# Kernel tuning notes

Hardware: AMD Instinct MI355X
Metric: run time of the kernel (lower is better)

## Reference

```python
import jax, jax.numpy as jnp
import numpy as np

N_NODES = 100000
N_EDGES = 1200000
F_IN, F_HID, F_OUT = 128, 64, 40


def gcn_conv(x, W, b, src, dst, n):
    # PyG GCNConv: h = x @ W; add self-loops; symmetric norm; scatter-add; + bias
    h = x @ W  # [N, F]
    loops = jnp.arange(n)
    s = jnp.concatenate([src, loops])
    d = jnp.concatenate([dst, loops])
    deg = jnp.zeros((n,), x.dtype).at[d].add(jnp.asarray(1.0, x.dtype))
    dis = jax.lax.rsqrt(deg)  # deg >= 1 thanks to self-loops
    norm = dis[s] * dis[d]  # [E+N]
    msg = h[s] * norm[:, None]  # gather + scale
    out = jnp.zeros((n, h.shape[1]), x.dtype).at[d].add(msg)  # scatter-add
    return out + b


def setup_inputs() -> dict:
    key = jax.random.key(0)
    ks = jax.random.split(key, 8)
    sc = lambda f: 1.0 / np.sqrt(f)
    return {
        "x": jax.random.normal(ks[0], (N_NODES, F_IN), jnp.float32),
        "edge_index": jax.random.randint(ks[1], (2, N_EDGES), 0, N_NODES, jnp.int64),
        "W1": jax.random.normal(ks[2], (F_IN, F_HID), jnp.float32) * sc(F_IN),
        "b1": jnp.zeros((F_HID,), jnp.float32),
        "W2": jax.random.normal(ks[3], (F_HID, F_HID), jnp.float32) * sc(F_HID),
        "b2": jnp.zeros((F_HID,), jnp.float32),
        "W3": jax.random.normal(ks[4], (F_HID, F_OUT), jnp.float32) * sc(F_HID),
        "b3": jnp.zeros((F_OUT,), jnp.float32),
    }


def reference(x, edge_index, W1, b1, W2, b2, W3, b3):
    src, dst = edge_index[0], edge_index[1]
    n = x.shape[0]
    h = jax.nn.relu(gcn_conv(x, W1, b1, src, dst, n))  # dropout is identity (eval)
    h = jax.nn.relu(gcn_conv(h, W2, b2, src, dst, n))
    out = gcn_conv(h, W3, b3, src, dst, n)
    return jax.nn.log_softmax(out, axis=1)
```

## Files before the change

### kernel.cpp

```cpp
#include <hip/hip_runtime.h>
#include <math.h>


static inline int cdiv(long a, int b) { return (int)((a + b - 1) / b); }

__device__ __forceinline__ unsigned short f2bf(float f) {
    unsigned u = __float_as_uint(f);
    u += 0x7fffu + ((u >> 16) & 1u);
    return (unsigned short)(u >> 16);
}
__device__ __forceinline__ float bf2f(unsigned short b) {
    return __uint_as_float(((unsigned)b) << 16);
}

typedef float floatx2 __attribute__((ext_vector_type(2)));
__device__ __forceinline__ float4 fp8x4_f(unsigned u) {
    floatx2 lo = __builtin_amdgcn_cvt_pk_f32_fp8(u, false);
    floatx2 hi = __builtin_amdgcn_cvt_pk_f32_fp8(u, true);
    float4 r; r.x = lo[0]; r.y = lo[1]; r.z = hi[0]; r.w = hi[1];
    return r;
}
__device__ __forceinline__ unsigned f_fp8x4(float4 v) {
    unsigned r = 0;
    r = __builtin_amdgcn_cvt_pk_fp8_f32(v.x, v.y, r, false);
    r = __builtin_amdgcn_cvt_pk_fp8_f32(v.z, v.w, r, true);
    return r;
}

#define RSH 9
#define RNODES 512
#define GB 1024
#define NBMAX 256
#define SMASK 0x1FFFF
#define PSLACK (RNODES * 16)

__global__ __launch_bounds__(256)
void k_bhist(const int* __restrict__ dst, int* __restrict__ bh,
             int E, int NB, int EPB) {
    __shared__ int bcnt[NBMAX];
    const int tid = threadIdx.x, blk = blockIdx.x;
    for (int i = tid; i < NB; i += 256) bcnt[i] = 0;
    __syncthreads();
    const int e1 = min(E, (blk + 1) * EPB);
    for (int e = blk * EPB + tid; e < e1; e += 256)
        atomicAdd(&bcnt[dst[e] >> RSH], 1);
    __syncthreads();
    for (int i = tid; i < NB; i += 256) bh[i * GB + blk] = bcnt[i];
}

__global__ __launch_bounds__(256)
void k_bscatter(const int* __restrict__ src, const int* __restrict__ dst,
                const int* __restrict__ eoff, int* __restrict__ ebuf,
                int E, int NB, int EPB) {
    __shared__ int cur[NBMAX];
    const int tid = threadIdx.x, blk = blockIdx.x;
    for (int i = tid; i < NB; i += 256) cur[i] = eoff[i * GB + blk];
    __syncthreads();
    const int e1 = min(E, (blk + 1) * EPB);
    for (int e = blk * EPB + tid; e < e1; e += 256) {
        int d = dst[e];
        int s = src[e];
        int pos = atomicAdd(&cur[d >> RSH], 1);
        ebuf[pos] = ((d & (RNODES - 1)) << 17) | s;
    }
}

__global__ __launch_bounds__(1024)
void k_csr(const int* __restrict__ ebuf, const int* __restrict__ eoff,
           uint2* __restrict__ rpd, float* __restrict__ dis,
           unsigned int* __restrict__ esrcb, int N, int E, int NB) {
    __shared__ int cnt[RNODES];
    __shared__ int cur[RNODES];
    __shared__ int sm[1024];
    const int tid = threadIdx.x, b = blockIdx.x;
    const int node0 = b << RSH;
    const int bb = eoff[b * GB];
    const int be = (b + 1 == NB) ? E : eoff[(b + 1) * GB];
    const int pbase = ((bb + 15) & ~15) + b * PSLACK;

    if (tid < RNODES) cnt[tid] = 0;
    __syncthreads();
    for (int e = bb + tid; e < be; e += 1024)
        atomicAdd(&cnt[ebuf[e] >> 17], 1);
    __syncthreads();

    int v  = (tid < RNODES) ? cnt[tid] : 0;
    int pv = (v + 15) & ~15;
    sm[tid] = pv;
    __syncthreads();
    for (int off = 1; off < RNODES; off <<= 1) {
        int t = (tid >= off) ? sm[tid - off] : 0;
        __syncthreads();
        sm[tid] += t;
        __syncthreads();
    }
    if (tid < RNODES) {
        int excl = sm[tid] - pv;
        cur[tid] = pbase + excl;
        int node = node0 + tid;
        if (node < N) {
            rpd[node] = make_uint2((unsigned)(pbase + excl), (unsigned)((v + 15) >> 4));
            dis[node] = rsqrtf(1.0f + (float)v);
        }
    }
    __syncthreads();
    const int ptot = sm[RNODES - 1];

    const unsigned ZOFF = (unsigned)N << 6;
    for (int k = tid; k < ptot; k += 1024) esrcb[pbase + k] = ZOFF;
    __syncthreads();

    for (int e = bb + tid; e < be; e += 1024) {
        int ev = ebuf[e];
        int slot = atomicAdd(&cur[ev >> 17], 1);
        esrcb[slot] = (unsigned)(ev & SMASK) << 6;
    }
}

#define SCAN_B 1024
__global__ void k_scan1(const int* __restrict__ cnt, int* __restrict__ rp,
                        int* __restrict__ bsum, int n, char* __restrict__ zbase,
                        int N) {
    __shared__ int sm[SCAN_B];
    const int tid = threadIdx.x;
    const int gid = blockIdx.x * SCAN_B + tid;
    if (blockIdx.x == 0 && tid < 16)
        ((unsigned*)(zbase + (size_t)N * 64))[tid] = 0;
    int v = (gid < n) ? cnt[gid] : 0;
    sm[tid] = v;
    __syncthreads();
    for (int off = 1; off < SCAN_B; off <<= 1) {
        int t = (tid >= off) ? sm[tid - off] : 0;
        __syncthreads();
        sm[tid] += t;
        __syncthreads();
    }
    if (gid < n) rp[gid] = sm[tid] - v;
    if (tid == SCAN_B - 1) bsum[blockIdx.x] = sm[tid];
}

__global__ void k_scan2(int* __restrict__ bsum, int nb) {
    __shared__ int sm[SCAN_B];
    const int tid = threadIdx.x;
    int v = (tid < nb) ? bsum[tid] : 0;
    sm[tid] = v;
    __syncthreads();
    for (int off = 1; off < SCAN_B; off <<= 1) {
        int t = (tid >= off) ? sm[tid - off] : 0;
        __syncthreads();
        sm[tid] += t;
        __syncthreads();
    }
    if (tid < nb) bsum[tid] = sm[tid] - v;
}

__global__ void k_scan3(int* __restrict__ rp, const int* __restrict__ bsum, int n, int E) {
    const int gid = blockIdx.x * SCAN_B + threadIdx.x;
    if (gid < n) rp[gid] += bsum[gid / SCAN_B];
    if (gid == n) rp[n] = E;
}

__device__ __forceinline__ void fma4(float a, const float4& w, float4& acc) {
    acc.x = fmaf(a, w.x, acc.x);
    acc.y = fmaf(a, w.y, acc.y);
    acc.z = fmaf(a, w.z, acc.z);
    acc.w = fmaf(a, w.w, acc.w);
}

template<int K, bool BF16IN, int MINW>
__global__ __launch_bounds__(256, MINW)
void k_gemm_lds(const void* __restrict__ Xv, const float* __restrict__ W,
                const float* __restrict__ dis, void* __restrict__ Hout, int N) {
    constexpr int KP = K + 4;
    __shared__ float xs[64 * KP];
    __shared__ float wsh[K * 64];
    const int tid = threadIdx.x;
    const int tx = tid & 15;
    const int ty = tid >> 4;
    const int row0 = blockIdx.x * 64;

    {
        const float4* Wg = (const float4*)W;
        float4* Wl = (float4*)wsh;
#pragma unroll
        for (int i = 0; i < K * 16 / 256; ++i)
            Wl[i * 256 + tid] = Wg[i * 256 + tid];
    }
    {
        constexpr int F4 = K / 4;
        for (int i = tid; i < 64 * F4; i += 256) {
            int r = i / F4, c = i - r * F4;
            int gr = min(row0 + r, N - 1);
            float4 v;
            if (BF16IN) {
                ushort4 u = *(const ushort4*)((const unsigned short*)Xv + (size_t)gr * K + c * 4);
                v.x = bf2f(u.x); v.y = bf2f(u.y); v.z = bf2f(u.z); v.w = bf2f(u.w);
            } else {
                v = *(const float4*)((const float*)Xv + (size_t)gr * K + c * 4);
            }
            *(float4*)(xs + r * KP + c * 4) = v;
        }
    }
    __syncthreads();

    float4 acc0 = {0.f, 0.f, 0.f, 0.f};
    float4 acc1 = {0.f, 0.f, 0.f, 0.f};
    float4 acc2 = {0.f, 0.f, 0.f, 0.f};
    float4 acc3 = {0.f, 0.f, 0.f, 0.f};

    const float* xr0 = xs + (ty * 4 + 0) * KP;
    const float* xr1 = xs + (ty * 4 + 1) * KP;
    const float* xr2 = xs + (ty * 4 + 2) * KP;
    const float* xr3 = xs + (ty * 4 + 3) * KP;

#pragma unroll 2
    for (int k = 0; k < K; k += 4) {
        float4 w0 = *(const float4*)(wsh + (k + 0) * 64 + tx * 4);
        float4 w1 = *(const float4*)(wsh + (k + 1) * 64 + tx * 4);
        float4 w2 = *(const float4*)(wsh + (k + 2) * 64 + tx * 4);
        float4 w3 = *(const float4*)(wsh + (k + 3) * 64 + tx * 4);
        float4 xa = *(const float4*)(xr0 + k);
        float4 xb = *(const float4*)(xr1 + k);
        float4 xc = *(const float4*)(xr2 + k);
        float4 xd = *(const float4*)(xr3 + k);

        fma4(xa.x, w0, acc0); fma4(xa.y, w1, acc0); fma4(xa.z, w2, acc0); fma4(xa.w, w3, acc0);
        fma4(xb.x, w0, acc1); fma4(xb.y, w1, acc1); fma4(xb.z, w2, acc1); fma4(xb.w, w3, acc1);
        fma4(xc.x, w0, acc2); fma4(xc.y, w1, acc2); fma4(xc.z, w2, acc2); fma4(xc.w, w3, acc2);
        fma4(xd.x, w0, acc3); fma4(xd.y, w1, acc3); fma4(xd.z, w2, acc3); fma4(xd.w, w3, acc3);
    }

    const int r = row0 + ty * 4;
#pragma unroll
    for (int i = 0; i < 4; ++i) {
        if (r + i >= N) break;
        float4 a = (i == 0) ? acc0 : (i == 1) ? acc1 : (i == 2) ? acc2 : acc3;
        float d = dis[r + i];
        a.x *= d; a.y *= d; a.z *= d; a.w *= d;
        unsigned o = f_fp8x4(a);
        *(unsigned*)((unsigned char*)Hout + (size_t)(r + i) * 64 + tx * 4) = o;
    }
}

template<int MODE>
__global__ __launch_bounds__(256, 8)
void k_agg(const unsigned char* __restrict__ Hs8, const float* __restrict__ dis,
           const uint2* __restrict__ rpd, const unsigned int* __restrict__ esrcb,
           const float* __restrict__ bias, void* __restrict__ A, int N) {
    const int wave = threadIdx.x >> 6;
    const int lane = threadIdx.x & 63;
    const int node = blockIdx.x * (blockDim.x >> 6) + wave;
    if (node >= N) return;
    const int q    = lane >> 4;
    const unsigned foff = (lane & 15) * 4;

    const uint2 pd = rpd[node];
    const char* base = (const char*)Hs8;
    float4 acc = {0.f, 0.f, 0.f, 0.f};
    unsigned e = pd.x + q * 4;
    for (unsigned it = 0; it < pd.y; ++it, e += 16) {
        uint4 ov = *(const uint4*)(esrcb + e);
        unsigned u0 = *(const unsigned*)(base + (ov.x + foff));
        unsigned u1 = *(const unsigned*)(base + (ov.y + foff));
        unsigned u2 = *(const unsigned*)(base + (ov.z + foff));
        unsigned u3 = *(const unsigned*)(base + (ov.w + foff));
        float4 h0 = fp8x4_f(u0);
        float4 h1 = fp8x4_f(u1);
        float4 h2 = fp8x4_f(u2);
        float4 h3 = fp8x4_f(u3);
        acc.x += (h0.x + h1.x) + (h2.x + h3.x);
        acc.y += (h0.y + h1.y) + (h2.y + h3.y);
        acc.z += (h0.z + h1.z) + (h2.z + h3.z);
        acc.w += (h0.w + h1.w) + (h2.w + h3.w);
    }
    acc.x += __shfl_xor(acc.x, 16, 64);
    acc.y += __shfl_xor(acc.y, 16, 64);
    acc.z += __shfl_xor(acc.z, 16, 64);
    acc.w += __shfl_xor(acc.w, 16, 64);
    acc.x += __shfl_xor(acc.x, 32, 64);
    acc.y += __shfl_xor(acc.y, 32, 64);
    acc.z += __shfl_xor(acc.z, 32, 64);
    acc.w += __shfl_xor(acc.w, 32, 64);

    if (lane < 16) {
        const float dd = dis[node];
        unsigned shv = *(const unsigned*)(Hs8 + (size_t)node * 64 + lane * 4);
        float4 sh = fp8x4_f(shv);
        float4 v;
        v.x = (acc.x + sh.x) * dd;
        v.y = (acc.y + sh.y) * dd;
        v.z = (acc.z + sh.z) * dd;
        v.w = (acc.w + sh.w) * dd;
        float4 bv = ((const float4*)bias)[lane];
        v.x = fmaxf(v.x + bv.x, 0.f);
        v.y = fmaxf(v.y + bv.y, 0.f);
        v.z = fmaxf(v.z + bv.z, 0.f);
        v.w = fmaxf(v.w + bv.w, 0.f);
        if (MODE == 1) {
            v.x *= dd; v.y *= dd; v.z *= dd; v.w *= dd;
        }
        ushort4 o;
        o.x = f2bf(v.x); o.y = f2bf(v.y); o.z = f2bf(v.z); o.w = f2bf(v.w);
        *(ushort4*)((unsigned short*)A + (size_t)node * 64 + lane * 4) = o;
    }
}

__global__ __launch_bounds__(256, 4)
void k_zgemm(const unsigned short* __restrict__ A2s, const float* __restrict__ W,
             unsigned char* __restrict__ Z8, int N, int npw) {
    const int wid  = blockIdx.x * (blockDim.x >> 6) + (threadIdx.x >> 6);
    const int lane = threadIdx.x & 63;
    const int cl   = (lane < 40) ? lane : 0;

    float w[64];
#pragma unroll
    for (int k = 0; k < 64; ++k) w[k] = W[k * 40 + cl];

    const int n0 = wid * npw;
    const int n1 = min(n0 + npw, N);
    for (int node = n0; node < n1; ++node) {
        const int un = __builtin_amdgcn_readfirstlane(node);
        const uint4* xr = (const uint4*)(A2s + (size_t)un * 64);
        float acc = 0.0f;
#pragma unroll
        for (int j = 0; j < 8; ++j) {
            uint4 u = xr[j];
            acc = fmaf(__uint_as_float(u.x << 16),          w[8 * j + 0], acc);
            acc = fmaf(__uint_as_float(u.x & 0xffff0000u),  w[8 * j + 1], acc);
            acc = fmaf(__uint_as_float(u.y << 16),          w[8 * j + 2], acc);
            acc = fmaf(__uint_as_float(u.y & 0xffff0000u),  w[8 * j + 3], acc);
            acc = fmaf(__uint_as_float(u.z << 16),          w[8 * j + 4], acc);
            acc = fmaf(__uint_as_float(u.z & 0xffff0000u),  w[8 * j + 5], acc);
            acc = fmaf(__uint_as_float(u.w << 16),          w[8 * j + 6], acc);
            acc = fmaf(__uint_as_float(u.w & 0xffff0000u),  w[8 * j + 7], acc);
        }
        unsigned p = __builtin_amdgcn_cvt_pk_fp8_f32(acc, acc, 0u, false);
        unsigned char byte = (lane < 40) ? (unsigned char)(p & 0xFFu) : (unsigned char)0;
        Z8[(size_t)node * 64 + lane] = byte;
    }
}

__global__ __launch_bounds__(256, 8)
void k_aggz(const unsigned char* __restrict__ Z8, const float* __restrict__ dis,
            const uint2* __restrict__ rpd, const unsigned int* __restrict__ esrcb,
            const float* __restrict__ b3, float* __restrict__ out, int N) {
    const int wave = threadIdx.x >> 6;
    const int lane = threadIdx.x & 63;
    const int node = blockIdx.x * (blockDim.x >> 6) + wave;
    if (node >= N) return;
    const int q    = lane >> 4;
    const int f4   = lane & 15;
    const unsigned foff = f4 * 4;

    const uint2 pd = rpd[node];
    const char* base = (const char*)Z8;
    float4 acc = {0.f, 0.f, 0.f, 0.f};
    unsigned e = pd.x + q * 4;
    for (unsigned it = 0; it < pd.y; ++it, e += 16) {
        uint4 ov = *(const uint4*)(esrcb + e);
        unsigned u0 = *(const unsigned*)(base + (ov.x + foff));
        unsigned u1 = *(const unsigned*)(base + (ov.y + foff));
        unsigned u2 = *(const unsigned*)(base + (ov.z + foff));
        unsigned u3 = *(const unsigned*)(base + (ov.w + foff));
        float4 h0 = fp8x4_f(u0);
        float4 h1 = fp8x4_f(u1);
        float4 h2 = fp8x4_f(u2);
        float4 h3 = fp8x4_f(u3);
        acc.x += (h0.x + h1.x) + (h2.x + h3.x);
        acc.y += (h0.y + h1.y) + (h2.y + h3.y);
        acc.z += (h0.z + h1.z) + (h2.z + h3.z);
        acc.w += (h0.w + h1.w) + (h2.w + h3.w);
    }
    acc.x += __shfl_xor(acc.x, 16, 64);
    acc.y += __shfl_xor(acc.y, 16, 64);
    acc.z += __shfl_xor(acc.z, 16, 64);
    acc.w += __shfl_xor(acc.w, 16, 64);
    acc.x += __shfl_xor(acc.x, 32, 64);
    acc.y += __shfl_xor(acc.y, 32, 64);
    acc.z += __shfl_xor(acc.z, 32, 64);
    acc.w += __shfl_xor(acc.w, 32, 64);

    const float dd = dis[node];
    unsigned shv = *(const unsigned*)(Z8 + (size_t)node * 64 + f4 * 4);
    float4 sh = fp8x4_f(shv);
    float4 bv = {0.f, 0.f, 0.f, 0.f};
    if (f4 < 10) bv = ((const float4*)b3)[f4];
    float4 v;
    v.x = (acc.x + sh.x) * dd + bv.x;
    v.y = (acc.y + sh.y) * dd + bv.y;
    v.z = (acc.z + sh.z) * dd + bv.z;
    v.w = (acc.w + sh.w) * dd + bv.w;

    float m = (f4 < 10) ? fmaxf(fmaxf(v.x, v.y), fmaxf(v.z, v.w)) : -INFINITY;
#pragma unroll
    for (int o = 1; o < 16; o <<= 1) m = fmaxf(m, __shfl_xor(m, o, 64));
    float es = (f4 < 10)
        ? expf(v.x - m) + expf(v.y - m) + expf(v.z - m) + expf(v.w - m) : 0.f;
#pragma unroll
    for (int o = 1; o < 16; o <<= 1) es += __shfl_xor(es, o, 64);

    if (lane < 10) {
        float ls = logf(es);
        float4 o4;
        o4.x = v.x - m - ls;
        o4.y = v.y - m - ls;
        o4.z = v.z - m - ls;
        o4.w = v.w - m - ls;
        *(float4*)(out + (size_t)node * 40 + lane * 4) = o4;
    }
}

extern "C" void kernel_launch(void* const* d_in, const int* in_sizes, int n_in,
                              void* d_out, int out_size, void* d_ws, size_t ws_size,
                              hipStream_t stream) {
    const float* x  = (const float*)d_in[0];
    const int*   ei = (const int*)d_in[1];
    const float* W1 = (const float*)d_in[2];
    const float* b1 = (const float*)d_in[3];
    const float* W2 = (const float*)d_in[4];
    const float* b2 = (const float*)d_in[5];
    const float* W3 = (const float*)d_in[6];
    const float* b3 = (const float*)d_in[7];
    float* out = (float*)d_out;

    const int N = in_sizes[0] / 128;
    const int E = in_sizes[1] / 2;
    const int* src = ei;
    const int* dst = ei + E;

    const int NB   = cdiv(N, RNODES);
    const int EPB  = cdiv(E, GB);
    const int nscan = NB * GB;
    const size_t esz = (size_t)E + (size_t)(NB + 2) * PSLACK + 64;

    char* ws = (char*)d_ws;
    char* buf0  = ws;                         ws += (size_t)(N + 1) * 64;
    char* buf1  = ws;                         ws += (size_t)N * 128;
    unsigned* esrcb = (unsigned*)ws;          ws += esz * sizeof(int);
    uint2* rpd  = (uint2*)ws;                 ws += (size_t)N * sizeof(uint2);
    int*   bsum  = (int*)ws;                  ws += (size_t)SCAN_B * sizeof(int);
    float* dis   = (float*)ws;                ws += (size_t)N * sizeof(float);
    int*   bh    = (int*)ws;                  ws += (size_t)nscan * sizeof(int);
    int*   eoff  = (int*)ws;                  ws += (size_t)(nscan + 1) * sizeof(int);
    int*   ebuf  = (int*)(ws);                ws += (size_t)E * sizeof(int);

    const int B = 256;
    const int nbs = cdiv(nscan, SCAN_B);

    k_bhist<<<GB, B, 0, stream>>>(dst, bh, E, NB, EPB);
    k_scan1<<<nbs, SCAN_B, 0, stream>>>(bh, eoff, bsum, nscan, buf0, N);
    k_scan2<<<1, SCAN_B, 0, stream>>>(bsum, nbs);
    k_scan3<<<cdiv(nscan + 1, SCAN_B), SCAN_B, 0, stream>>>(eoff, bsum, nscan, E);
    k_bscatter<<<GB, B, 0, stream>>>(src, dst, eoff, ebuf, E, NB, EPB);
    k_csr<<<NB, 1024, 0, stream>>>(ebuf, eoff, rpd, dis, esrcb, N, E, NB);

    k_gemm_lds<128, false, 2><<<cdiv(N, 64), B, 0, stream>>>(x, W1, dis, buf0, N);
    k_agg<0><<<cdiv(N, 4), B, 0, stream>>>((const unsigned char*)buf0, dis, rpd, esrcb,
                                           b1, buf1, N);

    k_gemm_lds<64, true, 4><<<cdiv(N, 64), B, 0, stream>>>(buf1, W2, dis, buf0, N);
    k_agg<1><<<cdiv(N, 4), B, 0, stream>>>((const unsigned char*)buf0, dis, rpd, esrcb,
                                           b2, buf1, N);

    const int NW = 8192;
    const int npw = cdiv(N, NW);
    k_zgemm<<<NW / 4, B, 0, stream>>>((const unsigned short*)buf1, W3,
                                      (unsigned char*)buf0, N, npw);
    k_aggz<<<cdiv(N, 4), B, 0, stream>>>((const unsigned char*)buf0, dis, rpd, esrcb,
                                         b3, out, N);
}
```

Before: 305.4 us.

## Replace FP32 FMA GEMMs with bf16 MFMA kernel shared across all three layers

Swaps the scalar-FMA LDS GEMM and the per-wave register GEMM for a single templated kernel that converts X and a transposed W to bf16 in LDS and computes 64-row tiles with 16x16x32 bf16 MFMA instructions. The third layer's 40-column GEMM now uses the same kernel, zero-padding W to 64 columns and writing fp8 outputs byte-wise. This aims to cut the FP32 ALU cost of the dense transforms. In exchange, layer-1 inputs are rounded to bf16, and the outputs are written as scattered single bytes rather than packed words.

```diff
diff --git a/kernel.cpp b/kernel.cpp
--- a/kernel.cpp
+++ b/kernel.cpp
@@ -14,17 +14,16 @@
 }
 
 typedef float floatx2 __attribute__((ext_vector_type(2)));
+typedef short bf16x8  __attribute__((ext_vector_type(8)));
+typedef float f32x4   __attribute__((ext_vector_type(4)));
 __device__ __forceinline__ float4 fp8x4_f(unsigned u) {
     floatx2 lo = __builtin_amdgcn_cvt_pk_f32_fp8(u, false);
     floatx2 hi = __builtin_amdgcn_cvt_pk_f32_fp8(u, true);
     float4 r; r.x = lo[0]; r.y = lo[1]; r.z = hi[0]; r.w = hi[1];
     return r;
 }
-__device__ __forceinline__ unsigned f_fp8x4(float4 v) {
-    unsigned r = 0;
-    r = __builtin_amdgcn_cvt_pk_fp8_f32(v.x, v.y, r, false);
-    r = __builtin_amdgcn_cvt_pk_fp8_f32(v.z, v.w, r, true);
-    return r;
+__device__ __forceinline__ unsigned char f_fp8(float v) {
+    return (unsigned char)(__builtin_amdgcn_cvt_pk_fp8_f32(v, v, 0u, false) & 0xFFu);
 }
 
 #define RSH 9
@@ -160,85 +159,77 @@
     if (gid == n) rp[n] = E;
 }
 
-__device__ __forceinline__ void fma4(float a, const float4& w, float4& acc) {
-    acc.x = fmaf(a, w.x, acc.x);
-    acc.y = fmaf(a, w.y, acc.y);
-    acc.z = fmaf(a, w.z, acc.z);
-    acc.w = fmaf(a, w.w, acc.w);
-}
-
-template<int K, bool BF16IN, int MINW>
-__global__ __launch_bounds__(256, MINW)
-void k_gemm_lds(const void* __restrict__ Xv, const float* __restrict__ W,
-                const float* __restrict__ dis, void* __restrict__ Hout, int N) {
-    constexpr int KP = K + 4;
-    __shared__ float xs[64 * KP];
-    __shared__ float wsh[K * 64];
+template<int K, bool BF16IN, int WCOLS, bool DIS>
+__global__ __launch_bounds__(256, 4)
+void k_mgemm(const void* __restrict__ Xv, const float* __restrict__ W,
+             const float* __restrict__ dis, unsigned char* __restrict__ Hout, int N) {
+    constexpr int KP = K + 8;
+    __shared__ short xs[64 * KP];
+    __shared__ short wt[64 * KP];
     const int tid = threadIdx.x;
-    const int tx = tid & 15;
-    const int ty = tid >> 4;
+    const int wv  = tid >> 6;
+    const int l   = tid & 63;
     const int row0 = blockIdx.x * 64;
 
-    {
-        const float4* Wg = (const float4*)W;
-        float4* Wl = (float4*)wsh;
+    for (int idx = tid; idx < K * 64; idx += 256) {
+        int k = idx >> 6, n = idx & 63;
+        float v;
+        if (WCOLS == 64) v = W[k * 64 + n];
+        else             v = (n < WCOLS) ? W[k * WCOLS + n] : 0.f;
+        wt[n * KP + k] = (short)f2bf(v);
+    }
+    if (BF16IN) {
+        constexpr int C4 = K / 4;
+        for (int idx = tid; idx < 64 * C4; idx += 256) {
+            int r = idx / C4, c = idx % C4;
+            int gr = min(row0 + r, N - 1);
+            ushort4 u = *(const ushort4*)((const unsigned short*)Xv + (size_t)gr * K + c * 4);
+            *(ushort4*)(&xs[r * KP + c * 4]) = u;
+        }
+    } else {
+        constexpr int C4 = K / 4;
+        for (int idx = tid; idx < 64 * C4; idx += 256) {
+            int r = idx / C4, c = idx % C4;
+            int gr = min(row0 + r, N - 1);
+            float4 v = *(const float4*)((const float*)Xv + (size_t)gr * K + c * 4);
+            ushort4 u;
+            u.x = f2bf(v.x); u.y = f2bf(v.y); u.z = f2bf(v.z); u.w = f2bf(v.w);
+            *(ushort4*)(&xs[r * KP + c * 4]) = u;
+        }
+    }
+    __syncthreads();
+
+    f32x4 acc0 = {0.f, 0.f, 0.f, 0.f};
+    f32x4 acc1 = {0.f, 0.f, 0.f, 0.f};
+    f32x4 acc2 = {0.f, 0.f, 0.f, 0.f};
+    f32x4 acc3 = {0.f, 0.f, 0.f, 0.f};
+    const int arow = wv * 16 + (l & 15);
+    const int koffl = (l >> 4) * 8;
+
 #pragma unroll
-        for (int i = 0; i < K * 16 / 256; ++i)
-            Wl[i * 256 + tid] = Wg[i * 256 + tid];
-    }
-    {
-        constexpr int F4 = K / 4;
-        for (int i = tid; i < 64 * F4; i += 256) {
-            int r = i / F4, c = i - r * F4;
-            int gr = min(row0 + r, N - 1);
-            float4 v;
-            if (BF16IN) {
-                ushort4 u = *(const ushort4*)((const unsigned short*)Xv + (size_t)gr * K + c * 4);
-                v.x = bf2f(u.x); v.y = bf2f(u.y); v.z = bf2f(u.z); v.w = bf2f(u.w);
-            } else {
-                v = *(const float4*)((const float*)Xv + (size_t)gr * K + c * 4);
-            }
-            *(float4*)(xs + r * KP + c * 4) = v;
+    for (int ks = 0; ks < K; ks += 32) {
+        bf16x8 a  = *(const bf16x8*)(&xs[arow * KP + ks + koffl]);
+        bf16x8 b0 = *(const bf16x8*)(&wt[( 0 + (l & 15)) * KP + ks + koffl]);
+        bf16x8 b1 = *(const bf16x8*)(&wt[(16 + (l & 15)) * KP + ks + koffl]);
+        bf16x8 b2 = *(const bf16x8*)(&wt[(32 + (l & 15)) * KP + ks + koffl]);
+        bf16x8 b3 = *(const bf16x8*)(&wt[(48 + (l & 15)) * KP + ks + koffl]);
+        acc0 = __builtin_amdgcn_mfma_f32_16x16x32_bf16(a, b0, acc0, 0, 0, 0);
+        acc1 = __builtin_amdgcn_mfma_f32_16x16x32_bf16(a, b1, acc1, 0, 0, 0);
+        acc2 = __builtin_amdgcn_mfma_f32_16x16x32_bf16(a, b2, acc2, 0, 0, 0);
+        acc3 = __builtin_amdgcn_mfma_f32_16x16x32_bf16(a, b3, acc3, 0, 0, 0);
+    }
+
+#pragma unroll
+    for (int j = 0; j < 4; ++j) {
+        int r = row0 + wv * 16 + ((l >> 4) << 2) + j;
+        if (r < N) {
+            float dd = DIS ? dis[r] : 1.0f;
+            unsigned char* rowp = Hout + (size_t)r * 64 + (l & 15);
+            rowp[0]  = f_fp8(acc0[j] * dd);
+            rowp[16] = f_fp8(acc1[j] * dd);
+            rowp[32] = f_fp8(acc2[j] * dd);
+            rowp[48] = f_fp8(acc3[j] * dd);
         }
-    }
-    __syncthreads();
-
-    float4 acc0 = {0.f, 0.f, 0.f, 0.f};
-    float4 acc1 = {0.f, 0.f, 0.f, 0.f};
-    float4 acc2 = {0.f, 0.f, 0.f, 0.f};
-    float4 acc3 = {0.f, 0.f, 0.f, 0.f};
-
-    const float* xr0 = xs + (ty * 4 + 0) * KP;
-    const float* xr1 = xs + (ty * 4 + 1) * KP;
-    const float* xr2 = xs + (ty * 4 + 2) * KP;
-    const float* xr3 = xs + (ty * 4 + 3) * KP;
-
-#pragma unroll 2
-    for (int k = 0; k < K; k += 4) {
-        float4 w0 = *(const float4*)(wsh + (k + 0) * 64 + tx * 4);
-        float4 w1 = *(const float4*)(wsh + (k + 1) * 64 + tx * 4);
-        float4 w2 = *(const float4*)(wsh + (k + 2) * 64 + tx * 4);
-        float4 w3 = *(const float4*)(wsh + (k + 3) * 64 + tx * 4);
-        float4 xa = *(const float4*)(xr0 + k);
-        float4 xb = *(const float4*)(xr1 + k);
-        float4 xc = *(const float4*)(xr2 + k);
-        float4 xd = *(const float4*)(xr3 + k);
-
-        fma4(xa.x, w0, acc0); fma4(xa.y, w1, acc0); fma4(xa.z, w2, acc0); fma4(xa.w, w3, acc0);
-        fma4(xb.x, w0, acc1); fma4(xb.y, w1, acc1); fma4(xb.z, w2, acc1); fma4(xb.w, w3, acc1);
-        fma4(xc.x, w0, acc2); fma4(xc.y, w1, acc2); fma4(xc.z, w2, acc2); fma4(xc.w, w3, acc2);
-        fma4(xd.x, w0, acc3); fma4(xd.y, w1, acc3); fma4(xd.z, w2, acc3); fma4(xd.w, w3, acc3);
-    }
-
-    const int r = row0 + ty * 4;
-#pragma unroll
-    for (int i = 0; i < 4; ++i) {
-        if (r + i >= N) break;
-        float4 a = (i == 0) ? acc0 : (i == 1) ? acc1 : (i == 2) ? acc2 : acc3;
-        float d = dis[r + i];
-        a.x *= d; a.y *= d; a.z *= d; a.w *= d;
-        unsigned o = f_fp8x4(a);
-        *(unsigned*)((unsigned char*)Hout + (size_t)(r + i) * 64 + tx * 4) = o;
     }
 }
 
@@ -305,41 +296,6 @@
     }
 }
 
-__global__ __launch_bounds__(256, 4)
-void k_zgemm(const unsigned short* __restrict__ A2s, const float* __restrict__ W,
-             unsigned char* __restrict__ Z8, int N, int npw) {
-    const int wid  = blockIdx.x * (blockDim.x >> 6) + (threadIdx.x >> 6);
-    const int lane = threadIdx.x & 63;
-    const int cl   = (lane < 40) ? lane : 0;
-
-    float w[64];
-#pragma unroll
-    for (int k = 0; k < 64; ++k) w[k] = W[k * 40 + cl];
-
-    const int n0 = wid * npw;
-    const int n1 = min(n0 + npw, N);
-    for (int node = n0; node < n1; ++node) {
-        const int un = __builtin_amdgcn_readfirstlane(node);
-        const uint4* xr = (const uint4*)(A2s + (size_t)un * 64);
-        float acc = 0.0f;
-#pragma unroll
-        for (int j = 0; j < 8; ++j) {
-            uint4 u = xr[j];
-            acc = fmaf(__uint_as_float(u.x << 16),          w[8 * j + 0], acc);
-            acc = fmaf(__uint_as_float(u.x & 0xffff0000u),  w[8 * j + 1], acc);
-            acc = fmaf(__uint_as_float(u.y << 16),          w[8 * j + 2], acc);
-            acc = fmaf(__uint_as_float(u.y & 0xffff0000u),  w[8 * j + 3], acc);
-            acc = fmaf(__uint_as_float(u.z << 16),          w[8 * j + 4], acc);
-            acc = fmaf(__uint_as_float(u.z & 0xffff0000u),  w[8 * j + 5], acc);
-            acc = fmaf(__uint_as_float(u.w << 16),          w[8 * j + 6], acc);
-            acc = fmaf(__uint_as_float(u.w & 0xffff0000u),  w[8 * j + 7], acc);
-        }
-        unsigned p = __builtin_amdgcn_cvt_pk_fp8_f32(acc, acc, 0u, false);
-        unsigned char byte = (lane < 40) ? (unsigned char)(p & 0xFFu) : (unsigned char)0;
-        Z8[(size_t)node * 64 + lane] = byte;
-    }
-}
-
 __global__ __launch_bounds__(256, 8)
 void k_aggz(const unsigned char* __restrict__ Z8, const float* __restrict__ dis,
             const uint2* __restrict__ rpd, const unsigned int* __restrict__ esrcb,
@@ -446,6 +402,7 @@
 
     const int B = 256;
     const int nbs = cdiv(nscan, SCAN_B);
+    const int ngb = cdiv(N, 64);
 
     k_bhist<<<GB, B, 0, stream>>>(dst, bh, E, NB, EPB);
     k_scan1<<<nbs, SCAN_B, 0, stream>>>(bh, eoff, bsum, nscan, buf0, N);
@@ -454,18 +411,18 @@
     k_bscatter<<<GB, B, 0, stream>>>(src, dst, eoff, ebuf, E, NB, EPB);
     k_csr<<<NB, 1024, 0, stream>>>(ebuf, eoff, rpd, dis, esrcb, N, E, NB);
 
-    k_gemm_lds<128, false, 2><<<cdiv(N, 64), B, 0, stream>>>(x, W1, dis, buf0, N);
+    k_mgemm<128, false, 64, true><<<ngb, B, 0, stream>>>(x, W1, dis,
+                                                         (unsigned char*)buf0, N);
     k_agg<0><<<cdiv(N, 4), B, 0, stream>>>((const unsigned char*)buf0, dis, rpd, esrcb,
                                            b1, buf1, N);
 
-    k_gemm_lds<64, true, 4><<<cdiv(N, 64), B, 0, stream>>>(buf1, W2, dis, buf0, N);
+    k_mgemm<64, true, 64, true><<<ngb, B, 0, stream>>>(buf1, W2, dis,
+                                                       (unsigned char*)buf0, N);
     k_agg<1><<<cdiv(N, 4), B, 0, stream>>>((const unsigned char*)buf0, dis, rpd, esrcb,
                                            b2, buf1, N);
 
-    const int NW = 8192;
-    const int npw = cdiv(N, NW);
-    k_zgemm<<<NW / 4, B, 0, stream>>>((const unsigned short*)buf1, W3,
-                                      (unsigned char*)buf0, N, npw);
+    k_mgemm<64, true, 40, false><<<ngb, B, 0, stream>>>(buf1, W3, dis,
+                                                        (unsigned char*)buf0, N);
     k_aggz<<<cdiv(N, 4), B, 0, stream>>>((const unsigned char*)buf0, dis, rpd, esrcb,
                                          b3, out, N);
 }
```

Measured after the change: 281.0 us. 1.09x faster.
